# Optimization experiments

Measured on AMD Instinct MI355X. Metric: run time of the kernel, lower is better.

Reference implementation:

```python
import jax, jax.numpy as jnp
from jax import lax
import numpy as np

B, IMG_H, IMG_W = 8, 256, 512
NUM_CLASSES, P = 20, 32
SCALE, TOPK, IOU_THR = 32.0, 100, 0.5


def conv2d(x, w, b, stride=1, pad=1):
    y = lax.conv_general_dilated(x, w, (stride, stride), [(pad, pad), (pad, pad)],
                                 dimension_numbers=('NCHW', 'OIHW', 'NCHW'))
    return y + b[None, :, None, None]


def bilinear_resize(img, out_h, out_w):
    # img: [..., H, W]; torch F.interpolate(mode='bilinear', align_corners=False)
    H, W = img.shape[-2], img.shape[-1]
    def idx_w(n_in, n_out):
        src = (jnp.arange(n_out, dtype=jnp.float32) + 0.5) * (n_in / n_out) - 0.5
        src = jnp.clip(src, 0.0, n_in - 1)
        i0 = jnp.floor(src).astype(jnp.int32)
        i1 = jnp.minimum(i0 + 1, n_in - 1)
        return i0, i1, src - i0.astype(jnp.float32)
    y0, y1, wy = idx_w(H, out_h)
    x0, x1, wx = idx_w(W, out_w)
    top = img[..., y0, :] * (1.0 - wy)[:, None] + img[..., y1, :] * wy[:, None]
    return top[..., x0] * (1.0 - wx) + top[..., x1] * wx


def generate_anchors(fh, fw):
    ys = (jnp.arange(fh, dtype=jnp.float32) + 0.5) * (IMG_H / fh)
    xs = (jnp.arange(fw, dtype=jnp.float32) + 0.5) * (IMG_W / fw)
    cy, cx = jnp.meshgrid(ys, xs, indexing='ij')
    h = SCALE / 2
    return jnp.stack([cx - h, cy - h, cx + h, cy + h], -1).reshape(-1, 4)


def delta_to_boxes(anchors, deltas):
    a_c = (anchors[:, :2] + anchors[:, 2:]) / 2
    a_wh = anchors[:, 2:] - anchors[:, :2]
    pc = a_c + deltas[..., :2] * a_wh
    pwh = a_wh * jnp.exp(deltas[..., 2:])
    return jnp.concatenate([pc - pwh / 2, pc + pwh / 2], -1)


def nms_single(boxes, scores, labels):
    # torchvision batched_nms: offset boxes per label, greedy NMS, return kept idxs
    N = boxes.shape[0]
    off = labels.astype(boxes.dtype) * (jnp.max(boxes) + 1.0)
    b = boxes + off[:, None]
    order = jnp.argsort(-scores)
    bs = b[order]
    area = (bs[:, 2] - bs[:, 0]) * (bs[:, 3] - bs[:, 1])
    lt = jnp.maximum(bs[:, None, :2], bs[None, :, :2])
    rb = jnp.minimum(bs[:, None, 2:], bs[None, :, 2:])
    wh = jnp.clip(rb - lt, 0.0)
    inter = wh[..., 0] * wh[..., 1]
    iou = inter / (area[:, None] + area[None, :] - inter + 1e-9)
    idxs = jnp.arange(N)
    def body(i, suppressed):
        keep_i = jnp.logical_not(suppressed[i])
        row = (iou[i] > IOU_THR) & (idxs > i)
        return jnp.where(keep_i, suppressed | row, suppressed)
    suppressed = lax.fori_loop(0, N, body, jnp.zeros(N, bool))
    keep_mask = ~suppressed
    rank = jnp.cumsum(keep_mask) - 1
    slots = jnp.where(keep_mask & (rank < TOPK), rank, TOPK)
    out = jnp.full(TOPK + 1, -1, jnp.int32).at[slots].set(order.astype(jnp.int32))
    return out[:TOPK]


def setup_inputs():
    key = jax.random.key(0)
    ks = jax.random.split(key, 17)
    def cw(k, o, i, kh, kw_):
        return jax.random.normal(k, (o, i, kh, kw_), jnp.float32) / np.sqrt(i * kh * kw_)
    return {
        'images': jax.random.normal(ks[0], (B, 3, IMG_H, IMG_W), jnp.float32),
        'w1': cw(ks[1], 64, 3, 3, 3),   'b1': jnp.zeros(64, jnp.float32),
        'w2': cw(ks[2], 128, 64, 3, 3), 'b2': jnp.zeros(128, jnp.float32),
        'w3': cw(ks[3], 256, 128, 3, 3),'b3': jnp.zeros(256, jnp.float32),
        'pw1': cw(ks[4], 256, 256, 3, 3), 'pb1': jnp.zeros(256, jnp.float32),
        'pw2': cw(ks[5], P, 256, 1, 1),   'pb2': jnp.zeros(P, jnp.float32),
        'cw_': cw(ks[6], NUM_CLASSES + 1, 256, 3, 3), 'cb': jnp.zeros(NUM_CLASSES + 1, jnp.float32),
        'bw': cw(ks[7], 4, 256, 3, 3),  'bb': jnp.zeros(4, jnp.float32),
        'kw': cw(ks[8], P, 256, 3, 3),  'kb': jnp.zeros(P, jnp.float32),
    }


def reference(images, w1, b1, w2, b2, w3, b3, pw1, pb1, pw2, pb2, cw_, cb, bw, bb, kw, kb):
    x = jax.nn.relu(conv2d(images, w1, b1, stride=2))
    x = jax.nn.relu(conv2d(x, w2, b2, stride=2))
    feat = jax.nn.relu(conv2d(x, w3, b3, stride=2))          # [B,256,32,64]
    proto = conv2d(jax.nn.relu(conv2d(feat, pw1, pb1)), pw2, pb2, pad=0)  # [B,P,32,64]
    fh, fw = feat.shape[2], feat.shape[3]
    def head(w, b, c):
        return conv2d(feat, w, b).transpose(0, 2, 3, 1).reshape(B, -1, c)
    cls = head(cw_, cb, NUM_CLASSES + 1)     # [B,N,C+1]
    box = head(bw, bb, 4)                    # [B,N,4]
    coef = head(kw, kb, P)                   # [B,N,P]
    anchors = generate_anchors(fh, fw)       # [N,4]
    probs = jax.nn.softmax(cls, -1)[..., :-1]
    scores = probs.max(-1)
    labels = probs.argmax(-1).astype(jnp.int32)
    boxes = delta_to_boxes(anchors, box)     # [B,N,4]
    keep = jax.vmap(nms_single)(boxes, scores, labels)   # [B,100], -1 pad
    valid = keep >= 0
    ki = jnp.clip(keep, 0)
    take = lambda a: jnp.take_along_axis(a, ki[..., None] if a.ndim == 3 else ki, axis=1)
    boxes_k = take(boxes) * valid[..., None]
    scores_k = take(scores) * valid
    labels_k = jnp.where(valid, take(labels), 0)
    coef_k = jnp.take_along_axis(coef, ki[..., None], axis=1)   # [B,100,P]
    m = jax.nn.sigmoid(jnp.einsum('bkp,bphw->bkhw', coef_k, proto))
    masks = bilinear_resize(m, IMG_H, IMG_W) > 0.5
    masks = masks & valid[..., None, None]
    return boxes_k, scores_k, labels_k, masks, valid
```

## Files before the change

### kernel.cpp

```cpp
#include <hip/hip_runtime.h>
#include <hip/hip_bf16.h>
#include <math.h>

#define BB 8
#define NCLS 21
#define NANCH 2048
#define TOPK_N 100

static const size_t OFF_X1HI = 0;
static const size_t OFF_X1LO = 34344960;
static const size_t OFF_X2HI = 68689920;
static const size_t OFF_X2LO = 86261760;
static const size_t OFF_FTHI = 103833600;
static const size_t OFF_FTLO = 113025024;
static const size_t OFF_A2H  = 122223616;
static const size_t OFF_A2L  = 122371072;
static const size_t OFF_A3H  = 122518528;
static const size_t OFF_A3L  = 123108352;
static const size_t OFF_AHH  = 123698176;
static const size_t OFF_AHL  = 123993088;
static const size_t OFF_AP1H = 124288000;
static const size_t OFF_AP1L = 125467648;
static const size_t OFF_WTP2 = 126647296;
static const size_t OFF_BH   = 126680064;
static const size_t OFF_HOUT = 126680576;
static const size_t OFF_P1   = 130874880;
static const size_t OFF_PROTO= 147652096;
static const size_t OFF_BOXES= 149749248;
static const size_t OFF_SCORES=150011392;
static const size_t OFF_LABELS=150076928;
static const size_t OFF_KEEP = 154664448;
static const size_t OFF_MAXB = 154668032;

static const size_t OUT_BOXES  = 0;
static const size_t OUT_SCORES = 3200;
static const size_t OUT_LABELS = 4000;
static const size_t OUT_MASKS  = 4800;
static const size_t OUT_VALID  = 104862400;

typedef __attribute__((ext_vector_type(8))) short bf16x8;
typedef __attribute__((ext_vector_type(4))) float f32x4;

__device__ __forceinline__ unsigned encf(float f){
  unsigned u = __float_as_uint(f);
  return (u & 0x80000000u) ? ~u : (u | 0x80000000u);
}
__device__ __forceinline__ float decf(unsigned u){
  unsigned b = (u & 0x80000000u) ? (u & 0x7fffffffu) : ~u;
  return __uint_as_float(b);
}
__device__ __forceinline__ short f2bf(float f){
  __hip_bfloat16 h = __float2bfloat16(f);
  return *(short*)&h;
}
__device__ __forceinline__ float bf2f(short h){
  return __uint_as_float(((unsigned)(unsigned short)h) << 16);
}

template<int CIN,int COUT,int KK>
__device__ __forceinline__ void packw_body(int i, const float* __restrict__ w,
                                           float* __restrict__ wT){
  if (i >= CIN*KK*COUT) return;
  int co = i % COUT; int r = i / COUT;
  int ci = r / KK,  k = r % KK;
  wT[i] = w[(co*CIN + ci)*KK + k];
}

template<int CIN,int COUT>
__device__ __forceinline__ void packA_body(int i, const float* __restrict__ w,
                                           short* __restrict__ Ahi, short* __restrict__ Alo){
  constexpr int K = CIN*9;
  constexpr int KS = K/32;
  if (i >= COUT*K) return;
  int sub  = i & 7;
  int lane = (i >> 3) & 63;
  int rest = i >> 9;
  int ks = rest % KS;
  int mt = rest / KS;
  int m = mt*16 + (lane & 15);
  int k = ks*32 + (lane >> 4)*8 + sub;
  int tap = k / CIN, ci = k - tap*CIN;
  float v = w[(m*CIN + ci)*9 + tap];
  short h = f2bf(v);
  Ahi[i] = h;
  Alo[i] = f2bf(v - bf2f(h));
}

__device__ __forceinline__ void packAh_body(int i,
    const float* __restrict__ cw, const float* __restrict__ bw,
    const float* __restrict__ kw, const float* __restrict__ cb,
    const float* __restrict__ bb, const float* __restrict__ kb,
    short* __restrict__ Ahi, short* __restrict__ Alo, float* __restrict__ bh){
  if (i < 64){
    float v = 0.f;
    if (i < 21) v = cb[i]; else if (i < 25) v = bb[i-21]; else if (i < 57) v = kb[i-25];
    bh[i] = v;
  }
  if (i >= 64*2304) return;
  constexpr int KS = 72;
  int sub  = i & 7;
  int lane = (i >> 3) & 63;
  int rest = i >> 9;
  int ks = rest % KS;
  int mt = rest / KS;
  int m = mt*16 + (lane & 15);
  int k = ks*32 + (lane >> 4)*8 + sub;
  int tap = k >> 8, ci = k & 255;
  float v = 0.f;
  if (m < 21)      v = cw[(m*256 + ci)*9 + tap];
  else if (m < 25) v = bw[((m-21)*256 + ci)*9 + tap];
  else if (m < 57) v = kw[((m-25)*256 + ci)*9 + tap];
  short h = f2bf(v);
  Ahi[i] = h;
  Alo[i] = f2bf(v - bf2f(h));
}

__global__ __launch_bounds__(256) void megaprep(
    const float* __restrict__ images, const float* __restrict__ w1, const float* __restrict__ b1,
    const float* __restrict__ w2, short* __restrict__ a2h, short* __restrict__ a2l,
    const float* __restrict__ w3, short* __restrict__ a3h, short* __restrict__ a3l,
    const float* __restrict__ pw1, short* __restrict__ ap1h, short* __restrict__ ap1l,
    const float* __restrict__ cw, const float* __restrict__ bw, const float* __restrict__ kw,
    const float* __restrict__ cb, const float* __restrict__ bb, const float* __restrict__ kb,
    short* __restrict__ ahh, short* __restrict__ ahl, float* __restrict__ bh,
    const float* __restrict__ pw2, float* __restrict__ wTp2,
    short* __restrict__ x1hi, short* __restrict__ x1lo,
    short* __restrict__ x2hi, short* __restrict__ x2lo,
    short* __restrict__ fthi, short* __restrict__ ftlo,
    unsigned* __restrict__ maxb){
  __shared__ float sw[27*64];
  const int blk = blockIdx.x, tid = threadIdx.x;

  if (blk < 583){
    int i = blk*256 + tid;
    if (i < BB) maxb[i] = 0u;
    short *hi, *lo; int Hp, Wp, cell, bg;
    if (i < 49408){
      hi=x1hi; lo=x1lo; Hp=130; Wp=258; cell = i % 772; bg = i / 772;
    } else if (i < 99072){
      int j = i - 49408; hi=x2hi; lo=x2lo; Hp=66; Wp=130; cell = j % 388; bg = j / 388;
    } else if (i < 149248){
      int j = i - 99072; hi=fthi; lo=ftlo; Hp=34; Wp=66; cell = j % 196; bg = j / 196;
    } else return;
    int y, x;
    if (cell < Wp)        { y = 0;      x = cell; }
    else if (cell < 2*Wp) { y = Hp-1;   x = cell - Wp; }
    else { int r = cell - 2*Wp; y = 1 + (r>>1); x = (r&1) ? (Wp-1) : 0; }
    size_t ad = (((size_t)bg*Hp + y)*Wp + x)*8;
    bf16x8 z = (bf16x8){0,0,0,0,0,0,0,0};
    *(bf16x8*)(hi + ad) = z;
    *(bf16x8*)(lo + ad) = z;
    return;
  }
  if (blk < 4935){
    int lb = blk - 583;
    if (lb < 288)        packA_body<64,128>(lb*256+tid, w2, a2h, a2l);
    else if (lb < 1440)  packA_body<128,256>((lb-288)*256+tid, w3, a3h, a3l);
    else if (lb < 3744)  packA_body<256,256>((lb-1440)*256+tid, pw1, ap1h, ap1l);
    else if (lb < 4320)  packAh_body((lb-3744)*256+tid, cw,bw,kw,cb,bb,kb, ahh,ahl,bh);
    else                 packw_body<256,32,1>((lb-4320)*256+tid, pw2, wTp2);
    return;
  }

  const int cblk = blk - 4935;
  const int bxc = cblk & 63;
  const int co0 = ((cblk >> 6) & 3) * 16;
  const int b   = cblk >> 8;
  for (int idx = tid; idx < 1728; idx += 256){
    int r = idx >> 6, co = idx & 63;
    sw[idx] = w1[co*27 + r];
  }
  __syncthreads();

  const int g  = bxc*256 + tid;
  const int y  = g >> 7;
  const int x0 = (g & 127) << 1;

  float acc[16][2];
#pragma unroll
  for (int c=0;c<16;c++){
    float bv = b1[co0+c];
    acc[c][0] = bv; acc[c][1] = bv;
  }
  int   off[3][5];
  float msk[3][5];
#pragma unroll
  for (int kh=0;kh<3;kh++){
    int iy = y*2 - 1 + kh;
    bool okr = (iy >= 0) && (iy < 256);
    int ro = okr ? iy*512 : 0;
#pragma unroll
    for (int t=0;t<5;t++){
      int col = x0*2 - 1 + t;
      bool ok = okr && (col >= 0) && (col < 512);
      off[kh][t] = ok ? (ro + col) : 0;
      msk[kh][t] = ok ? 1.f : 0.f;
    }
  }
  const float* inb = images + (size_t)b*3*256*512;
  for (int ci=0; ci<3; ci++){
    const float* inc = inb + (size_t)ci*256*512;
    float v[3][5];
#pragma unroll
    for (int kh=0;kh<3;kh++)
#pragma unroll
      for (int t=0;t<5;t++)
        v[kh][t] = inc[off[kh][t]] * msk[kh][t];
    const float* wp = sw + ci*9*64 + co0;
#pragma unroll
    for (int kh=0;kh<3;kh++)
#pragma unroll
    for (int kw2=0;kw2<3;kw2++){
      const float* wq = wp + (kh*3+kw2)*64;
#pragma unroll
      for (int c=0;c<16;c++){
        float wv = wq[c];
        acc[c][0] = fmaf(wv, v[kh][2*0+kw2], acc[c][0]);
        acc[c][1] = fmaf(wv, v[kh][2*1+kw2], acc[c][1]);
      }
    }
  }
#pragma unroll
  for (int s=0;s<2;s++){
    short hv[16] __attribute__((aligned(16)));
    short lv[16] __attribute__((aligned(16)));
#pragma unroll
    for (int c=0;c<16;c++){
      float r = fmaxf(acc[c][s], 0.f);
      short h = f2bf(r);
      hv[c] = h;
      lv[c] = f2bf(r - bf2f(h));
    }
#pragma unroll
    for (int g2=0; g2<2; g2++){
      size_t ad = (((size_t)(b*8 + (co0>>3) + g2)*130 + (y+1))*258 + (x0+s+1))*8;
      *(bf16x8*)(x1hi + ad) = *(bf16x8*)(hv + g2*8);
      *(bf16x8*)(x1lo + ad) = *(bf16x8*)(lv + g2*8);
    }
  }
}

template<int CIN,int K,int M,int MW,int NW,int S,int IPH,int IPW,int NXB,
         bool SPLIT,bool STAGELO,bool STAGEREG,int EMODE,int OPH,int OPW>
__device__ __forceinline__ void cgemm_row_body(
    short* sB, int bxi, int byi, int bzi,
    const short* __restrict__ Ahi, const short* __restrict__ Alo,
    const short* __restrict__ Bhi, const short* __restrict__ Blo,
    const float* __restrict__ bias, float* __restrict__ outf,
    short* __restrict__ outhi, short* __restrict__ outlo){
  static_assert(CIN % 32 == 0, "CIN must be multiple of 32");
  constexpr int NT = 64*32;
  constexpr int KS = K/32;
  constexpr int CG = CIN/8;
  constexpr int SW  = 64*S + 2;
  constexpr int SWP = (S==2) ? (SW/2 + 1) : SW;
  constexpr int LOOFF = CG*((S==2)?2:1)*SWP*8;
  constexpr int NTH = NW*64;
  constexpr int NLD = (CG*SW + NTH - 1)/NTH;

  const int b    = bzi;
  const int oy   = bxi / NXB;
  const int xb   = (bxi % NXB) * 64;
  const int wave = threadIdx.x >> 6;
  const int lane = threadIdx.x & 63;
  const int lm = lane & 15, lq = lane >> 4;
  const int m0 = (byi * NW + wave) * (MW*16);
  const int tid = threadIdx.x;

  f32x4 acc[MW][4];
#pragma unroll
  for (int i=0;i<MW;i++)
#pragma unroll
    for (int j=0;j<4;j++) acc[i][j] = (f32x4){0.f,0.f,0.f,0.f};

  const short* Ah_l = Ahi + (size_t)lane*8;
  const short* Al_l = Alo + (size_t)lane*8;
  const int mt0 = m0 >> 4;
  const size_t plane = (size_t)IPH*IPW;
  const short* Bl0 = Blo + ((size_t)b*CG + lq)*plane*8;

  bf16x8 rh[STAGEREG ? NLD : 1];
  bf16x8 rl[(STAGEREG && SPLIT && STAGELO) ? NLD : 1];

  auto LOADS = [&](int iyv){
    const short* srch = Bhi + (((size_t)b*CG*IPH + iyv)*IPW + (size_t)(xb*S))*8;
#pragma unroll
    for (int t=0;t<NLD;t++){
      int c = tid + t*NTH;
      if (c < CG*SW){
        int g = c / SW, p = c - g*SW;
        rh[t] = *(const bf16x8*)(srch + ((size_t)g*plane + p)*8);
      }
    }
    if constexpr (SPLIT && STAGELO){
      const short* srcl = Blo + (((size_t)b*CG*IPH + iyv)*IPW + (size_t)(xb*S))*8;
#pragma unroll
      for (int t=0;t<NLD;t++){
        int c = tid + t*NTH;
        if (c < CG*SW){
          int g = c / SW, p = c - g*SW;
          rl[t] = *(const bf16x8*)(srcl + ((size_t)g*plane + p)*8);
        }
      }
    }
  };
  auto WRITES = [&](){
#pragma unroll
    for (int t=0;t<NLD;t++){
      int c = tid + t*NTH;
      if (c < CG*SW){
        int g = c / SW, p = c - g*SW;
        int dst = (S==2) ? ((g*2 + (p&1))*SWP + (p>>1)) : (g*SW + p);
        *(bf16x8*)(&sB[(size_t)dst*8]) = rh[t];
        if constexpr (SPLIT && STAGELO)
          *(bf16x8*)(&sB[LOOFF + (size_t)dst*8]) = rl[t];
      }
    }
  };

  if constexpr (STAGEREG){
    LOADS(oy*S);
    WRITES();
    __syncthreads();
  }

#pragma unroll 1
  for (int dy=0; dy<3; dy++){
    const int iy = oy*S + dy;
    if constexpr (STAGEREG){
      if (dy < 2) LOADS(oy*S + dy + 1);
    } else {
      __syncthreads();
      {
        const short* srch = Bhi + (((size_t)b*CG*IPH + iy)*IPW + (size_t)(xb*S))*8;
        for (int c = tid; c < CG*SW; c += NTH){
          int g = c / SW, p = c - g*SW;
          int dst = (S==2) ? ((g*2 + (p&1))*SWP + (p>>1)) : (g*SW + p);
          *(bf16x8*)(&sB[(size_t)dst*8]) =
            *(const bf16x8*)(srch + ((size_t)g*plane + p)*8);
        }
        if constexpr (SPLIT && STAGELO){
          const short* srcl = Blo + (((size_t)b*CG*IPH + iy)*IPW + (size_t)(xb*S))*8;
          for (int c = tid; c < CG*SW; c += NTH){
            int g = c / SW, p = c - g*SW;
            int dst = (S==2) ? ((g*2 + (p&1))*SWP + (p>>1)) : (g*SW + p);
            *(bf16x8*)(&sB[LOOFF + (size_t)dst*8]) =
              *(const bf16x8*)(srcl + ((size_t)g*plane + p)*8);
          }
        }
      }
      __syncthreads();
    }
#pragma unroll
    for (int dx=0; dx<3; dx++){
      const int tap = dy*3 + dx;
      const int ksb = tap*(CIN/32);
#pragma unroll
      for (int kc=0; kc<CIN; kc+=32){
        const int ks = ksb + (kc>>5);
        int ra[4];
#pragma unroll
        for (int j=0;j<4;j++){
          int pc = (j*16 + lm)*S + dx;
          ra[j] = (S==2) ? ((((kc>>3) + lq)*2 + (pc&1))*SWP + (pc>>1))
                         : (((kc>>3) + lq)*SW + pc);
        }
        bf16x8 ah[MW], bh_[4];
#pragma unroll
        for (int i=0;i<MW;i++)
          ah[i] = *(const bf16x8*)(Ah_l + ((size_t)(mt0+i)*KS + ks)*512);
#pragma unroll
        for (int j=0;j<4;j++)
          bh_[j] = *(const bf16x8*)(&sB[(size_t)ra[j]*8]);
        if constexpr (SPLIT){
          bf16x8 al[MW], bl_[4];
#pragma unroll
          for (int i=0;i<MW;i++)
            al[i] = *(const bf16x8*)(Al_l + ((size_t)(mt0+i)*KS + ks)*512);
          if constexpr (STAGELO){
#pragma unroll
            for (int j=0;j<4;j++)
              bl_[j] = *(const bf16x8*)(&sB[LOOFF + (size_t)ra[j]*8]);
          } else {
#pragma unroll
            for (int j=0;j<4;j++){
              size_t pix = (size_t)iy*IPW + (size_t)((xb + j*16 + lm)*S + dx);
              bl_[j] = *(const bf16x8*)(Bl0 + ((size_t)(kc>>3)*plane + pix)*8);
            }
          }
#pragma unroll
          for (int j=0;j<4;j++)
#pragma unroll
            for (int i=0;i<MW;i++)
              acc[i][j] = __builtin_amdgcn_mfma_f32_16x16x32_bf16(ah[i], bh_[j], acc[i][j], 0,0,0);
#pragma unroll
          for (int j=0;j<4;j++)
#pragma unroll
            for (int i=0;i<MW;i++)
              acc[i][j] = __builtin_amdgcn_mfma_f32_16x16x32_bf16(ah[i], bl_[j], acc[i][j], 0,0,0);
#pragma unroll
          for (int j=0;j<4;j++)
#pragma unroll
            for (int i=0;i<MW;i++)
              acc[i][j] = __builtin_amdgcn_mfma_f32_16x16x32_bf16(al[i], bh_[j], acc[i][j], 0,0,0);
        } else {
#pragma unroll
          for (int j=0;j<4;j++)
#pragma unroll
            for (int i=0;i<MW;i++)
              acc[i][j] = __builtin_amdgcn_mfma_f32_16x16x32_bf16(ah[i], bh_[j], acc[i][j], 0,0,0);
        }
      }
    }
    if constexpr (STAGEREG){
      if (dy < 2){
        __syncthreads();
        WRITES();
        __syncthreads();
      }
    }
  }

#pragma unroll
  for (int i=0;i<MW;i++){
#pragma unroll
    for (int r=0;r<4;r++){
      const int m = m0 + i*16 + lq*4 + r;
      const float bv = bias[m];
      if constexpr (EMODE == 0){
#pragma unroll
        for (int j=0;j<4;j++){
          const int ox = xb + j*16 + lm;
          float v = fmaxf(acc[i][j][r] + bv, 0.f);
          short h = f2bf(v);
          short l = f2bf(v - bf2f(h));
          size_t ad = ((((size_t)(b*(M/8) + (m>>3))*OPH + (oy+1))*OPW + (ox+1)))*8 + (m&7);
          outhi[ad] = h;
          outlo[ad] = l;
        }
      } else {
        float* cp = outf + ((size_t)b*M + m)*NT + oy*64 + lm;
#pragma unroll
        for (int j=0;j<4;j++){
          float v = acc[i][j][r] + bv;
          if constexpr (EMODE == 2) v = fmaxf(v, 0.f);
          cp[j*16] = v;
        }
      }
    }
  }
}

template<int CIN,int K,int M,int MW,int NW,int S,int IPH,int IPW,int NXB,
         bool SPLIT,bool STAGELO,bool STAGEREG,int EMODE,int OPH,int OPW>
__global__ __launch_bounds__(NW*64) void cgemm_row(
    const short* __restrict__ Ahi, const short* __restrict__ Alo,
    const short* __restrict__ Bhi, const short* __restrict__ Blo,
    const float* __restrict__ bias, float* __restrict__ outf,
    short* __restrict__ outhi, short* __restrict__ outlo){
  constexpr int CG = CIN/8;
  constexpr int SW  = 64*S + 2;
  constexpr int SWP = (S==2) ? (SW/2 + 1) : SW;
  constexpr int LOOFF = CG*((S==2)?2:1)*SWP*8;
  constexpr int BUFS = (SPLIT && STAGELO) ? 2 : 1;
  __shared__ __align__(16) short sB[BUFS*LOOFF];
  cgemm_row_body<CIN,K,M,MW,NW,S,IPH,IPW,NXB,SPLIT,STAGELO,STAGEREG,EMODE,OPH,OPW>(
      sB, blockIdx.x, blockIdx.y, blockIdx.z,
      Ahi, Alo, Bhi, Blo, bias, outf, outhi, outlo);
}

__device__ __forceinline__ void headsdec_body(
    short* sB, int oy, int b,
    const short* __restrict__ Ahi, const short* __restrict__ Alo,
    const short* __restrict__ Bhi, const short* __restrict__ Blo,
    const float* __restrict__ bias, float* __restrict__ hout,
    float* __restrict__ boxes, float* __restrict__ scores,
    int* __restrict__ labels, unsigned* __restrict__ maxb){
  constexpr int KS = 72;
  constexpr int CG = 32;
  constexpr int SW = 66;
  constexpr int IPH = 34, IPW = 66;
  constexpr int LOOFF = CG*SW*8;
  constexpr int NLD = (CG*SW + 255)/256;

  const int wave = threadIdx.x >> 6;
  const int lane = threadIdx.x & 63;
  const int lm = lane & 15, lq = lane >> 4;
  const int tid = threadIdx.x;

  f32x4 acc[4];
#pragma unroll
  for (int j=0;j<4;j++) acc[j] = (f32x4){0.f,0.f,0.f,0.f};

  const short* Ah_l = Ahi + (size_t)lane*8;
  const short* Al_l = Alo + (size_t)lane*8;
  const size_t plane = (size_t)IPH*IPW;

  bf16x8 rh[NLD], rl[NLD];
  auto HLOADS = [&](int iyv){
    const short* srch = Bhi + ((size_t)b*CG*IPH + iyv)*IPW*8;
    const short* srcl = Blo + ((size_t)b*CG*IPH + iyv)*IPW*8;
#pragma unroll
    for (int t=0;t<NLD;t++){
      int c = tid + t*256;
      if (c < CG*SW){
        int g = c / SW, p = c - g*SW;
        rh[t] = *(const bf16x8*)(srch + ((size_t)g*plane + p)*8);
        rl[t] = *(const bf16x8*)(srcl + ((size_t)g*plane + p)*8);
      }
    }
  };
  auto HWRITES = [&](){
#pragma unroll
    for (int t=0;t<NLD;t++){
      int c = tid + t*256;
      if (c < CG*SW){
        *(bf16x8*)(&sB[(size_t)c*8]) = rh[t];
        *(bf16x8*)(&sB[LOOFF + (size_t)c*8]) = rl[t];
      }
    }
  };

  HLOADS(oy);
  HWRITES();
  __syncthreads();

#pragma unroll 1
  for (int dy=0; dy<3; dy++){
    if (dy < 2) HLOADS(oy + dy + 1);
#pragma unroll
    for (int dx=0; dx<3; dx++){
      const int tap = dy*3 + dx;
      const int ksb = tap*8;
#pragma unroll
      for (int kc=0; kc<256; kc+=32){
        const int ks = ksb + (kc>>5);
        int ra[4];
#pragma unroll
        for (int j=0;j<4;j++) ra[j] = ((kc>>3) + lq)*SW + (j*16 + lm) + dx;
        bf16x8 bh_[4], bl_[4];
#pragma unroll
        for (int j=0;j<4;j++){
          bh_[j] = *(const bf16x8*)(&sB[(size_t)ra[j]*8]);
          bl_[j] = *(const bf16x8*)(&sB[LOOFF + (size_t)ra[j]*8]);
        }
        bf16x8 ah = *(const bf16x8*)(Ah_l + ((size_t)wave*KS + ks)*512);
        bf16x8 al = *(const bf16x8*)(Al_l + ((size_t)wave*KS + ks)*512);
#pragma unroll
        for (int j=0;j<4;j++)
          acc[j] = __builtin_amdgcn_mfma_f32_16x16x32_bf16(ah, bh_[j], acc[j], 0,0,0);
#pragma unroll
        for (int j=0;j<4;j++)
          acc[j] = __builtin_amdgcn_mfma_f32_16x16x32_bf16(ah, bl_[j], acc[j], 0,0,0);
#pragma unroll
        for (int j=0;j<4;j++)
          acc[j] = __builtin_amdgcn_mfma_f32_16x16x32_bf16(al, bh_[j], acc[j], 0,0,0);
      }
    }
    if (dy < 2){
      __syncthreads();
      HWRITES();
      __syncthreads();
    }
  }

  __syncthreads();
  float* sF = (float*)sB;
#pragma unroll
  for (int r=0;r<4;r++){
    const int m = wave*16 + lq*4 + r;
    const float bv = bias[m];
    float* cp = hout + ((size_t)b*64 + m)*NANCH + oy*64 + lm;
#pragma unroll
    for (int j=0;j<4;j++){
      float v = acc[j][r] + bv;
      cp[j*16] = v;
      sF[m*68 + j*16 + lm] = v;
    }
  }
  __syncthreads();

  if (tid < 64){
    const int n = oy*64 + tid;
    float l[NCLS];
    float M = -1e30f;
#pragma unroll
    for (int c=0;c<NCLS;c++){ l[c] = sF[c*68 + tid]; M = fmaxf(M, l[c]); }
    float denom = 0.f;
#pragma unroll
    for (int c=0;c<NCLS;c++) denom += expf(l[c]-M);
    float best = -1.f; int bi = 0;
#pragma unroll
    for (int c=0;c<NCLS-1;c++){
      float e = expf(l[c]-M);
      if (e > best){ best = e; bi = c; }
    }
    scores[(size_t)b*NANCH + n] = best/denom;
    labels[(size_t)b*NANCH + n] = bi;

    float dxv = sF[21*68 + tid], dyv = sF[22*68 + tid];
    float dwv = sF[23*68 + tid], dhv = sF[24*68 + tid];
    const int yy = n >> 6, xx = n & 63;
    float cx = (xx+0.5f)*8.f, cy = (yy+0.5f)*8.f;
    float px = cx + dxv*32.f, py = cy + dyv*32.f;
    float pw = 32.f*expf(dwv), ph = 32.f*expf(dhv);
    float x1 = px - 0.5f*pw, y1 = py - 0.5f*ph;
    float x2 = px + 0.5f*pw, y2 = py + 0.5f*ph;
    float* bo = boxes + ((size_t)b*NANCH + n)*4;
    bo[0]=x1; bo[1]=y1; bo[2]=x2; bo[3]=y2;
    float mx = fmaxf(fmaxf(x1,y1), fmaxf(x2,y2));
#pragma unroll
    for (int off=32; off>0; off>>=1) mx = fmaxf(mx, __shfl_down(mx, off));
    if (tid == 0) atomicMax(maxb + b, encf(mx));
  }
}

__global__ __launch_bounds__(256) void headpw1k(
    const short* __restrict__ ahh, const short* __restrict__ ahl,
    const short* __restrict__ ap1h,
    const short* __restrict__ fthi, const short* __restrict__ ftlo,
    const float* __restrict__ bh, const float* __restrict__ pb1,
    float* __restrict__ hout, float* __restrict__ p1,
    float* __restrict__ boxes, float* __restrict__ scores,
    int* __restrict__ labels, unsigned* __restrict__ maxb){
  __shared__ __align__(16) short smem[33792];
  const int bx = blockIdx.x, b = blockIdx.z;
  if (bx < 32){
    headsdec_body(smem, bx, b, ahh, ahl, fthi, ftlo, bh, hout,
                  boxes, scores, labels, maxb);
  } else {
    const int lx = bx - 32;
    cgemm_row_body<256,2304,256,2,4,1,34,66,1,false,false,true,2,1,1>(
        smem, lx & 31, lx >> 5, b, ap1h, ap1h, fthi, fthi, pb1, p1, nullptr, nullptr);
  }
}

__global__ void __launch_bounds__(1024) pw2nms(
    const float* __restrict__ p1, const float* __restrict__ wT,
    const float* __restrict__ biasp, float* __restrict__ proto,
    const float* __restrict__ scores, const float* __restrict__ boxes,
    const int* __restrict__ labels, const unsigned* __restrict__ maxb,
    int* __restrict__ keep, float* __restrict__ out){
  __shared__ float sc[NANCH];
  __shared__ int   id[NANCH];
  __shared__ float sbL[NANCH*4];
  __shared__ unsigned long long sup[32];
  __shared__ int s_keep[TOPK_N];
  __shared__ int s_next;
  const int bx = blockIdx.x, t = threadIdx.x;
  if (bx < 16){
    const int b  = bx >> 1;
    const int sp = (bx & 1)*1024 + t;
    float acc[32];
#pragma unroll
    for (int c=0;c<32;c++) acc[c] = biasp[c];
    const float* pb = p1 + (size_t)b*256*NANCH + sp;
    for (int ci=0;ci<256;ci++){
      float v = pb[(size_t)ci*NANCH];
      const float* wq = wT + ci*32;
#pragma unroll
      for (int c=0;c<32;c++) acc[c] = fmaf(v, wq[c], acc[c]);
    }
#pragma unroll
    for (int c=0;c<32;c++)
      proto[((size_t)b*32 + c)*NANCH + sp] = acc[c];
    return;
  }
  const int b = bx - 16;
  for (int i=t;i<NANCH;i+=1024){ sc[i]=scores[(size_t)b*NANCH+i]; id[i]=i; }
  if (t < 32) sup[t] = 0ull;
  __syncthreads();
  for (int k=2;k<=NANCH;k<<=1){
    for (int j=k>>1;j>0;j>>=1){
      for (int i=t;i<NANCH;i+=1024){
        int ixj = i ^ j;
        if (ixj > i){
          float sa=sc[i], sb_=sc[ixj]; int ia=id[i], ib=id[ixj];
          bool dir = ((i & k) == 0);
          bool before_ba = (sb_ > sa) || (sb_ == sa && ib < ia);
          if (before_ba == dir){ sc[i]=sb_; sc[ixj]=sa; id[i]=ib; id[ixj]=ia; }
        }
      }
      __syncthreads();
    }
  }
  float mboff = decf(maxb[b]) + 1.0f;
  for (int r=t;r<NANCH;r+=1024){
    int o = id[r];
    float off = (float)labels[(size_t)b*NANCH + o] * mboff;
    const float* bo = boxes + ((size_t)b*NANCH + o)*4;
    sbL[r*4]   = bo[0]+off; sbL[r*4+1] = bo[1]+off;
    sbL[r*4+2] = bo[2]+off; sbL[r*4+3] = bo[3]+off;
  }
  __syncthreads();
  int k = 0, i = 0;
  while (true){
    if (k >= TOPK_N) break;
    if (t < 64){
      unsigned long long avail = (t < 32) ? ~sup[t] : 0ull;
      const int wi = i >> 6;
      if ((int)t < wi) avail = 0ull;
      else if ((int)t == wi) avail &= (~0ull) << (i & 63);
      unsigned long long ball = __ballot(avail != 0ull);
      int nxt = -1;
      if (ball){
        int w0 = (int)__builtin_ctzll(ball);
        unsigned long long aw = __shfl(avail, w0);
        int b0 = (int)__builtin_ctzll(aw);
        nxt = (w0 << 6) + b0;
      }
      if (t == 0) s_next = nxt;
    }
    __syncthreads();
    i = s_next;
    if (i < 0) break;
    if (t == 0) s_keep[k] = id[i];
    k++;
    float x1 = sbL[i*4], y1 = sbL[i*4+1], x2 = sbL[i*4+2], y2 = sbL[i*4+3];
    float ai = (x2-x1)*(y2-y1);
    bool f0 = false, f1 = false;
    {
      int j = t;
      if (j > i){
        float bx1=sbL[j*4], by1=sbL[j*4+1], bx2=sbL[j*4+2], by2=sbL[j*4+3];
        float lx=fmaxf(x1,bx1), ly=fmaxf(y1,by1);
        float rx=fminf(x2,bx2), ry=fminf(y2,by2);
        float ww=fmaxf(rx-lx,0.f), hh=fmaxf(ry-ly,0.f);
        float inter = ww*hh;
        float aj = (bx2-bx1)*(by2-by1);
        f0 = (inter/(ai + aj - inter + 1e-9f)) > 0.5f;
      }
      j = t + 1024;
      if (j > i){
        float bx1=sbL[j*4], by1=sbL[j*4+1], bx2=sbL[j*4+2], by2=sbL[j*4+3];
        float lx=fmaxf(x1,bx1), ly=fmaxf(y1,by1);
        float rx=fminf(x2,bx2), ry=fminf(y2,by2);
        float ww=fmaxf(rx-lx,0.f), hh=fmaxf(ry-ly,0.f);
        float inter = ww*hh;
        float aj = (bx2-bx1)*(by2-by1);
        f1 = (inter/(ai + aj - inter + 1e-9f)) > 0.5f;
      }
    }
    unsigned long long b0m = __ballot(f0);
    unsigned long long b1m = __ballot(f1);
    if ((t & 63) == 0){
      sup[t >> 6]        |= b0m;
      sup[16 + (t >> 6)] |= b1m;
    }
    i++;
    __syncthreads();
  }
  __syncthreads();
  for (int r = t; r < TOPK_N; r += 1024){
    int kv = (r < k) ? s_keep[r] : -1;
    keep[b*TOPK_N + r] = kv;
    float valid = (kv >= 0) ? 1.f : 0.f;
    int kc = (kv < 0) ? 0 : kv;
    const float* bo = boxes + ((size_t)b*NANCH + kc)*4;
#pragma unroll
    for (int c=0;c<4;c++) out[OUT_BOXES + ((size_t)b*TOPK_N + r)*4 + c] = bo[c]*valid;
    out[OUT_SCORES + b*TOPK_N + r] = scores[(size_t)b*NANCH + kc]*valid;
    out[OUT_LABELS + b*TOPK_N + r] = (kv >= 0) ? (float)labels[(size_t)b*NANCH + kc] : 0.f;
    out[OUT_VALID  + b*TOPK_N + r] = valid;
  }
}

__global__ __launch_bounds__(256) void maskresize(const int* __restrict__ keep,
    const float* __restrict__ hout, const float* __restrict__ proto,
    float* __restrict__ out){
  const int b = blockIdx.x & 7, r = blockIdx.x >> 3;
  float* obase = out + OUT_MASKS + ((size_t)b*TOPK_N + r)*131072;
  int ki = keep[b*TOPK_N + r];
  if (ki < 0){
    float4 z = make_float4(0.f,0.f,0.f,0.f);
    for (int idx = threadIdx.x; idx < 32768; idx += 256)
      ((float4*)obase)[idx] = z;
    return;
  }
  __shared__ float cf[32];
  __shared__ float sm[NANCH];
  if (threadIdx.x < 32)
    cf[threadIdx.x] = hout[((size_t)b*64 + 25 + threadIdx.x)*NANCH + ki];
  __syncthreads();
  for (int s = threadIdx.x; s < NANCH; s += 256){
    float acc = 0.f;
#pragma unroll
    for (int p=0;p<32;p++) acc = fmaf(cf[p], proto[((size_t)b*32 + p)*NANCH + s], acc);
    sm[s] = 1.f/(1.f + expf(-acc));
  }
  __syncthreads();
  for (int pid = threadIdx.x; pid < 32768; pid += 256){
    const int y  = pid >> 7;
    const int x4 = (pid & 127) << 2;
    float sy = (y + 0.5f)*0.125f - 0.5f;
    sy = fminf(fmaxf(sy, 0.f), 31.f);
    int y0 = (int)floorf(sy);
    int y1 = min(y0+1, 31);
    float wy = sy - (float)y0;
    const float* r0 = sm + y0*64;
    const float* r1 = sm + y1*64;
    float res[4];
#pragma unroll
    for (int kk=0;kk<4;kk++){
      int x = x4 + kk;
      float sx = (x + 0.5f)*0.125f - 0.5f;
      sx = fminf(fmaxf(sx, 0.f), 63.f);
      int x0 = (int)floorf(sx);
      int x1 = min(x0+1, 63);
      float wx = sx - (float)x0;
      float t0 = r0[x0]*(1.f-wy) + r1[x0]*wy;
      float t1 = r0[x1]*(1.f-wy) + r1[x1]*wy;
      float v  = t0*(1.f-wx) + t1*wx;
      res[kk] = (v > 0.5f) ? 1.f : 0.f;
    }
    *(float4*)(obase + y*512 + x4) = make_float4(res[0], res[1], res[2], res[3]);
  }
}

extern "C" void kernel_launch(void* const* d_in, const int* in_sizes, int n_in,
                              void* d_out, int out_size, void* d_ws, size_t ws_size,
                              hipStream_t stream) {
  const float* images=(const float*)d_in[0];
  const float* w1=(const float*)d_in[1];  const float* b1=(const float*)d_in[2];
  const float* w2=(const float*)d_in[3];  const float* b2=(const float*)d_in[4];
  const float* w3=(const float*)d_in[5];  const float* b3=(const float*)d_in[6];
  const float* pw1=(const float*)d_in[7]; const float* pb1=(const float*)d_in[8];
  const float* pw2=(const float*)d_in[9]; const float* pb2=(const float*)d_in[10];
  const float* cw=(const float*)d_in[11]; const float* cb=(const float*)d_in[12];
  const float* bw=(const float*)d_in[13]; const float* bb=(const float*)d_in[14];
  const float* kw=(const float*)d_in[15]; const float* kb=(const float*)d_in[16];
  float* out = (float*)d_out;
  char* ws = (char*)d_ws;

  short* x1hi = (short*)(ws + OFF_X1HI);
  short* x1lo = (short*)(ws + OFF_X1LO);
  short* x2hi = (short*)(ws + OFF_X2HI);
  short* x2lo = (short*)(ws + OFF_X2LO);
  short* fthi = (short*)(ws + OFF_FTHI);
  short* ftlo = (short*)(ws + OFF_FTLO);
  short* a2h  = (short*)(ws + OFF_A2H);
  short* a2l  = (short*)(ws + OFF_A2L);
  short* a3h  = (short*)(ws + OFF_A3H);
  short* a3l  = (short*)(ws + OFF_A3L);
  short* ahh  = (short*)(ws + OFF_AHH);
  short* ahl  = (short*)(ws + OFF_AHL);
  short* ap1h = (short*)(ws + OFF_AP1H);
  short* ap1l = (short*)(ws + OFF_AP1L);
  float* wTp2 = (float*)(ws + OFF_WTP2);
  float* bh   = (float*)(ws + OFF_BH);
  float* hout = (float*)(ws + OFF_HOUT);
  float* p1   = (float*)(ws + OFF_P1);
  float* proto= (float*)(ws + OFF_PROTO);
  float* boxes= (float*)(ws + OFF_BOXES);
  float* scores=(float*)(ws + OFF_SCORES);
  int*   labels=(int*)  (ws + OFF_LABELS);
  int*   keep = (int*)  (ws + OFF_KEEP);
  unsigned* maxb = (unsigned*)(ws + OFF_MAXB);

  megaprep<<<dim3(6983), 256, 0, stream>>>(
      images, w1, b1, w2, a2h, a2l, w3, a3h, a3l, pw1, ap1h, ap1l,
      cw, bw, kw, cb, bb, kb, ahh, ahl, bh, pw2, wTp2,
      x1hi, x1lo, x2hi, x2lo, fthi, ftlo, maxb);

  cgemm_row<64,576,128,2,4,2,130,258,2,true,true,true,0,66,130>
      <<<dim3(128,1,BB), 256, 0, stream>>>(a2h, a2l, x1hi, x1lo, b2, nullptr, x2hi, x2lo);

  cgemm_row<128,1152,256,2,4,2,66,130,1,true,true,true,0,34,66>
      <<<dim3(32,2,BB), 256, 0, stream>>>(a3h, a3l, x2hi, x2lo, b3, nullptr, fthi, ftlo);

  headpw1k<<<dim3(96,1,BB), 256, 0, stream>>>(ahh, ahl, ap1h, fthi, ftlo,
                                              bh, pb1, hout, p1,
                                              boxes, scores, labels, maxb);

  pw2nms<<<dim3(24), 1024, 0, stream>>>(p1, wTp2, pb2, proto,
                                        scores, boxes, labels, maxb, keep, out);

  maskresize<<<dim3(800), 256, 0, stream>>>(keep, hout, proto, out);
}
```

Before: 836.1 us.

## Fuse proto 3x3 conv with 1x1 projection inside head kernel, drop p1 buffer

The proto-branch 3x3 conv (pw1) now runs per output row in a new body that keeps the 256-channel ReLU result in shared memory and immediately applies the 1x1 pw2 projection to 32 channels, writing proto directly. This removes the large p1 intermediate in global memory and takes pw2 out of the NMS kernel, which now launches only the 8 NMS blocks. Grid changes from 96 to 64 blocks per batch, with one row per block instead of the previous tiling. Tradeoffs: coarser work per block, fewer blocks, and the pw2 FMA loop now sits serially after the MFMA loop in the same block.

```diff
diff --git a/kernel.cpp b/kernel.cpp
--- a/kernel.cpp
+++ b/kernel.cpp
@@ -24,7 +24,6 @@
 static const size_t OFF_WTP2 = 126647296;
 static const size_t OFF_BH   = 126680064;
 static const size_t OFF_HOUT = 126680576;
-static const size_t OFF_P1   = 130874880;
 static const size_t OFF_PROTO= 147652096;
 static const size_t OFF_BOXES= 149749248;
 static const size_t OFF_SCORES=150011392;
@@ -615,12 +614,134 @@
   }
 }
 
+__device__ __forceinline__ void pw1pw2_body(
+    short* sB, int oy, int b,
+    const short* __restrict__ Aph, const short* __restrict__ Bhi,
+    const float* __restrict__ biasp, const float* __restrict__ wTp2,
+    const float* __restrict__ pb2, float* __restrict__ proto){
+  constexpr int KS = 72;
+  constexpr int CG = 32;
+  constexpr int SW = 66;
+  constexpr int IPH = 34, IPW = 66;
+  constexpr int NLD = (CG*SW + 255)/256;
+
+  const int wave = threadIdx.x >> 6;
+  const int lane = threadIdx.x & 63;
+  const int lm = lane & 15, lq = lane >> 4;
+  const int tid = threadIdx.x;
+  const int m0 = wave*64;
+  const int mt0 = m0 >> 4;
+
+  f32x4 acc[4][4];
+#pragma unroll
+  for (int i=0;i<4;i++)
+#pragma unroll
+    for (int j=0;j<4;j++) acc[i][j] = (f32x4){0.f,0.f,0.f,0.f};
+
+  const short* Ap_l = Aph + (size_t)lane*8;
+  const size_t plane = (size_t)IPH*IPW;
+
+  bf16x8 rh[NLD];
+  auto PLOADS = [&](int iyv){
+    const short* srch = Bhi + ((size_t)b*CG*IPH + iyv)*IPW*8;
+#pragma unroll
+    for (int t=0;t<NLD;t++){
+      int c = tid + t*256;
+      if (c < CG*SW){
+        int g = c / SW, p = c - g*SW;
+        rh[t] = *(const bf16x8*)(srch + ((size_t)g*plane + p)*8);
+      }
+    }
+  };
+  auto PWRITES = [&](){
+#pragma unroll
+    for (int t=0;t<NLD;t++){
+      int c = tid + t*256;
+      if (c < CG*SW)
+        *(bf16x8*)(&sB[(size_t)c*8]) = rh[t];
+    }
+  };
+
+  PLOADS(oy);
+  PWRITES();
+  __syncthreads();
+
+#pragma unroll 1
+  for (int dy=0; dy<3; dy++){
+    if (dy < 2) PLOADS(oy + dy + 1);
+#pragma unroll
+    for (int dx=0; dx<3; dx++){
+      const int tap = dy*3 + dx;
+      const int ksb = tap*8;
+#pragma unroll
+      for (int kc=0; kc<256; kc+=32){
+        const int ks = ksb + (kc>>5);
+        int ra[4];
+#pragma unroll
+        for (int j=0;j<4;j++) ra[j] = ((kc>>3) + lq)*SW + (j*16 + lm) + dx;
+        bf16x8 ah[4], bh_[4];
+#pragma unroll
+        for (int i=0;i<4;i++)
+          ah[i] = *(const bf16x8*)(Ap_l + ((size_t)(mt0+i)*KS + ks)*512);
+#pragma unroll
+        for (int j=0;j<4;j++)
+          bh_[j] = *(const bf16x8*)(&sB[(size_t)ra[j]*8]);
+#pragma unroll
+        for (int j=0;j<4;j++)
+#pragma unroll
+          for (int i=0;i<4;i++)
+            acc[i][j] = __builtin_amdgcn_mfma_f32_16x16x32_bf16(ah[i], bh_[j], acc[i][j], 0,0,0);
+      }
+    }
+    if (dy < 2){
+      __syncthreads();
+      PWRITES();
+      __syncthreads();
+    }
+  }
+
+  __syncthreads();
+  float* sF = (float*)sB;
+#pragma unroll
+  for (int i=0;i<4;i++){
+#pragma unroll
+    for (int r=0;r<4;r++){
+      const int m = m0 + i*16 + lq*4 + r;
+      const float bv = biasp[m];
+#pragma unroll
+      for (int j=0;j<4;j++)
+        sF[m*65 + j*16 + lm] = fmaxf(acc[i][j][r] + bv, 0.f);
+    }
+  }
+  __syncthreads();
+
+  const int sp = tid & 63;
+  const int c0 = (tid >> 6) * 8;
+  float a[8];
+#pragma unroll
+  for (int k=0;k<8;k++) a[k] = pb2[c0 + k];
+#pragma unroll 4
+  for (int ci=0; ci<256; ci++){
+    float v = sF[ci*65 + sp];
+    const float4 w0 = *(const float4*)(wTp2 + ci*32 + c0);
+    const float4 w1_ = *(const float4*)(wTp2 + ci*32 + c0 + 4);
+    a[0] = fmaf(v, w0.x, a[0]); a[1] = fmaf(v, w0.y, a[1]);
+    a[2] = fmaf(v, w0.z, a[2]); a[3] = fmaf(v, w0.w, a[3]);
+    a[4] = fmaf(v, w1_.x, a[4]); a[5] = fmaf(v, w1_.y, a[5]);
+    a[6] = fmaf(v, w1_.z, a[6]); a[7] = fmaf(v, w1_.w, a[7]);
+  }
+#pragma unroll
+  for (int k=0;k<8;k++)
+    proto[((size_t)b*32 + c0 + k)*NANCH + oy*64 + sp] = a[k];
+}
+
 __global__ __launch_bounds__(256) void headpw1k(
     const short* __restrict__ ahh, const short* __restrict__ ahl,
     const short* __restrict__ ap1h,
     const short* __restrict__ fthi, const short* __restrict__ ftlo,
     const float* __restrict__ bh, const float* __restrict__ pb1,
-    float* __restrict__ hout, float* __restrict__ p1,
+    const float* __restrict__ wTp2, const float* __restrict__ pb2,
+    float* __restrict__ hout, float* __restrict__ proto,
     float* __restrict__ boxes, float* __restrict__ scores,
     int* __restrict__ labels, unsigned* __restrict__ maxb){
   __shared__ __align__(16) short smem[33792];
@@ -629,15 +750,11 @@
     headsdec_body(smem, bx, b, ahh, ahl, fthi, ftlo, bh, hout,
                   boxes, scores, labels, maxb);
   } else {
-    const int lx = bx - 32;
-    cgemm_row_body<256,2304,256,2,4,1,34,66,1,false,false,true,2,1,1>(
-        smem, lx & 31, lx >> 5, b, ap1h, ap1h, fthi, fthi, pb1, p1, nullptr, nullptr);
-  }
-}
-
-__global__ void __launch_bounds__(1024) pw2nms(
-    const float* __restrict__ p1, const float* __restrict__ wT,
-    const float* __restrict__ biasp, float* __restrict__ proto,
+    pw1pw2_body(smem, bx - 32, b, ap1h, fthi, pb1, wTp2, pb2, proto);
+  }
+}
+
+__global__ void __launch_bounds__(1024) nmsk(
     const float* __restrict__ scores, const float* __restrict__ boxes,
     const int* __restrict__ labels, const unsigned* __restrict__ maxb,
     int* __restrict__ keep, float* __restrict__ out){
@@ -647,26 +764,7 @@
   __shared__ unsigned long long sup[32];
   __shared__ int s_keep[TOPK_N];
   __shared__ int s_next;
-  const int bx = blockIdx.x, t = threadIdx.x;
-  if (bx < 16){
-    const int b  = bx >> 1;
-    const int sp = (bx & 1)*1024 + t;
-    float acc[32];
-#pragma unroll
-    for (int c=0;c<32;c++) acc[c] = biasp[c];
-    const float* pb = p1 + (size_t)b*256*NANCH + sp;
-    for (int ci=0;ci<256;ci++){
-      float v = pb[(size_t)ci*NANCH];
-      const float* wq = wT + ci*32;
-#pragma unroll
-      for (int c=0;c<32;c++) acc[c] = fmaf(v, wq[c], acc[c]);
-    }
-#pragma unroll
-    for (int c=0;c<32;c++)
-      proto[((size_t)b*32 + c)*NANCH + sp] = acc[c];
-    return;
-  }
-  const int b = bx - 16;
+  const int b = blockIdx.x, t = threadIdx.x;
   for (int i=t;i<NANCH;i+=1024){ sc[i]=scores[(size_t)b*NANCH+i]; id[i]=i; }
   if (t < 32) sup[t] = 0ull;
   __syncthreads();
@@ -849,7 +947,6 @@
   float* wTp2 = (float*)(ws + OFF_WTP2);
   float* bh   = (float*)(ws + OFF_BH);
   float* hout = (float*)(ws + OFF_HOUT);
-  float* p1   = (float*)(ws + OFF_P1);
   float* proto= (float*)(ws + OFF_PROTO);
   float* boxes= (float*)(ws + OFF_BOXES);
   float* scores=(float*)(ws + OFF_SCORES);
@@ -868,12 +965,12 @@
   cgemm_row<128,1152,256,2,4,2,66,130,1,true,true,true,0,34,66>
       <<<dim3(32,2,BB), 256, 0, stream>>>(a3h, a3l, x2hi, x2lo, b3, nullptr, fthi, ftlo);
 
-  headpw1k<<<dim3(96,1,BB), 256, 0, stream>>>(ahh, ahl, ap1h, fthi, ftlo,
-                                              bh, pb1, hout, p1,
+  headpw1k<<<dim3(64,1,BB), 256, 0, stream>>>(ahh, ahl, ap1h, fthi, ftlo,
+                                              bh, pb1, wTp2, pb2,
+                                              hout, proto,
                                               boxes, scores, labels, maxb);
 
-  pw2nms<<<dim3(24), 1024, 0, stream>>>(p1, wTp2, pb2, proto,
-                                        scores, boxes, labels, maxb, keep, out);
+  nmsk<<<dim3(BB), 1024, 0, stream>>>(scores, boxes, labels, maxb, keep, out);
 
   maskresize<<<dim3(800), 256, 0, stream>>>(keep, hout, proto, out);
 }
```

Result: slower. 854.0 us (+2.1%).
